# Performance work log

Measured on AMD Instinct MI355X. Metric: run time of the kernel, lower is better.

The kernel has to match this reference:

```python
import jax, jax.numpy as jnp
import numpy as np

N = 50000   # nodes (single node type)
E = 200000  # edges per relation
R = 2       # relations (etypes)
D = 256     # in_dim == out_dim
H = 8       # heads
DK = D // H # 32
SQRT_DK = float(np.sqrt(DK))


def setup_inputs() -> dict:
    key = jax.random.key(0)
    ks = jax.random.split(key, 12)
    wsc = 1.0 / np.sqrt(D)   # linear-layer scale
    rsc = 1.0 / np.sqrt(DK)  # xavier-ish scale for relation tensors
    return {
        "x": jax.random.normal(ks[0], (N, D), jnp.float32),
        "src": jax.random.randint(ks[1], (R, E), 0, N, jnp.int32),
        "dst": jax.random.randint(ks[2], (R, E), 0, N, jnp.int32),
        "Wk": jax.random.normal(ks[3], (D, D), jnp.float32) * wsc,
        "bk": jnp.zeros((D,), jnp.float32),
        "Wq": jax.random.normal(ks[4], (D, D), jnp.float32) * wsc,
        "bq": jnp.zeros((D,), jnp.float32),
        "Wv": jax.random.normal(ks[5], (D, D), jnp.float32) * wsc,
        "bv": jnp.zeros((D,), jnp.float32),
        "Wa": jax.random.normal(ks[6], (D, D), jnp.float32) * wsc,
        "ba": jnp.zeros((D,), jnp.float32),
        "rel_pri": jnp.ones((R, H), jnp.float32),
        "rel_att": jax.random.normal(ks[7], (R, H, DK, DK), jnp.float32) * rsc,
        "rel_msg": jax.random.normal(ks[8], (R, H, DK, DK), jnp.float32) * rsc,
        "skip": jnp.ones((1,), jnp.float32),
    }


def reference(x, src, dst, Wk, bk, Wq, bq, Wv, bv, Wa, ba, rel_pri, rel_att, rel_msg, skip):
    # Per-type K/Q/V projections (single node type) -> [N,H,DK]
    k = (x @ Wk + bk).reshape(N, H, DK)
    q = (x @ Wq + bq).reshape(N, H, DK)
    v = (x @ Wv + bv).reshape(N, H, DK)

    # edge_attention: per-relation bmm transform of gathered src features
    key_t = jnp.einsum('rehd,rhdf->rehf', k[src], rel_att)   # [R,E,H,DK]
    val = jnp.einsum('rehd,rhdf->rehf', v[src], rel_msg)     # [R,E,H,DK]
    att = (q[dst] * key_t).sum(-1) * rel_pri[:, None, :] / SQRT_DK  # [R,E,H]

    # segment softmax over incoming edges per (relation, dst node)
    seg = (dst + N * jnp.arange(R, dtype=dst.dtype)[:, None]).reshape(-1)  # [R*E]
    att_f = att.reshape(R * E, H)
    m = jax.ops.segment_max(att_f, seg, num_segments=R * N)
    m = jnp.where(jnp.isfinite(m), m, 0.0)  # empty segments -> never gathered
    e = jnp.exp(att_f - m[seg])
    den = jax.ops.segment_sum(e, seg, num_segments=R * N)
    attn = e / den[seg]                                       # [R*E,H]

    # weighted-sum scatter aggregation, then cross_reducer='mean' over relations
    h = jax.ops.segment_sum(attn[:, :, None] * val.reshape(R * E, H, DK), seg,
                            num_segments=R * N)               # [R*N,H,DK]
    t = h.reshape(R, N, D).mean(axis=0)                        # [N,D]

    # skip-gated output projection (dropout inactive in eval, use_norm=False)
    alpha = jax.nn.sigmoid(skip[0])
    return (t @ Wa + ba) * alpha + x * (1.0 - alpha)
```

## Files before the change

### kernel.cpp

```cpp
#include <hip/hip_runtime.h>
#include <hip/hip_bf16.h>
#include <math.h>

#define NN 50000
#define EE 200000
#define DD 256
#define HH 8
#define DKK 32
#define NSEG (2 * NN)
#define SCAN_BLOCKS ((NSEG + 1023) / 1024)
#define MPAD 50048
#define LDQKV 1280
#define CAST_BLOCKS 12500

constexpr float RSQRT_DK = 0.17677669529663687f;

__device__ __forceinline__ float bf_lo(unsigned u) { return __uint_as_float(u << 16); }
__device__ __forceinline__ float bf_hi(unsigned u) { return __uint_as_float(u & 0xffff0000u); }
__device__ __forceinline__ unsigned short f2bf(float f) {
    unsigned u = __float_as_uint(f);
    return (unsigned short)((u + 0x7fffu + ((u >> 16) & 1u)) >> 16);
}

typedef __attribute__((ext_vector_type(8))) short bf16x8;
typedef __attribute__((ext_vector_type(4))) float f32x4;

#define GLDS16(g, l)                                                                   \
    __builtin_amdgcn_global_load_lds((const __attribute__((address_space(1))) unsigned int*)(g), \
                                     (__attribute__((address_space(3))) unsigned int*)(l), 16, 0, 0)

__global__ void prep_kernel(const float* __restrict__ x, unsigned short* __restrict__ xb,
                            const float* __restrict__ Wq, const float* __restrict__ Wk,
                            const float* __restrict__ Wv, const float* __restrict__ bq,
                            const float* __restrict__ bk, const float* __restrict__ bv,
                            const float* __restrict__ rel_att, const float* __restrict__ rel_msg,
                            const float* __restrict__ Wa, unsigned short* __restrict__ wa_t,
                            unsigned short* __restrict__ Wt, float* __restrict__ bb) {
    if (blockIdx.x < CAST_BLOCKS) {
        const size_t i = ((size_t)blockIdx.x * 256 + threadIdx.x) * 4;
        float4 v = *(const float4*)&x[i];
        ushort4 o;
        o.x = f2bf(v.x); o.y = f2bf(v.y); o.z = f2bf(v.z); o.w = f2bf(v.w);
        *(ushort4*)&xb[i] = o;
        return;
    }
    const int n = blockIdx.x - CAST_BLOCKS, kk = threadIdx.x;
    if (n >= 1280) {
        const int nn = n - 1280;
        wa_t[(size_t)nn * 256 + kk] = f2bf(Wa[(size_t)kk * 256 + nn]);
        return;
    }
    if (n < 256) {
        Wt[(size_t)n * 256 + kk] = f2bf(Wq[(size_t)kk * 256 + n]);
        if (kk == 0) bb[n] = bq[n];
        return;
    }
    const int sec = (n - 256) >> 8;
    const int c = (n - 256) & 255;
    const int h = c >> 5, f = c & 31;
    const float* W    = (sec < 2) ? Wk : Wv;
    const float* bsrc = (sec < 2) ? bk : bv;
    const float* T = ((sec < 2) ? rel_att : rel_msg)
                   + (size_t)(sec & 1) * HH * DKK * DKK + (size_t)h * DKK * DKK + f;
    const float* wrow = &W[(size_t)kk * 256 + h * 32];
    float s = 0.f;
    #pragma unroll
    for (int d = 0; d < 32; ++d) s += wrow[d] * T[(size_t)d * 32];
    Wt[(size_t)n * 256 + kk] = f2bf(s);
    if (kk == 0) {
        float sb = 0.f;
        for (int d = 0; d < 32; ++d) sb += bsrc[h * 32 + d] * T[(size_t)d * 32];
        bb[n] = sb;
    }
}

__global__ __launch_bounds__(256) void mfma_gemm(
        const unsigned short* __restrict__ A, const unsigned short* __restrict__ Bt,
        const float* __restrict__ bias,
        unsigned short* __restrict__ Cbf, float* __restrict__ Cf,
        int M, int ldc, const float* __restrict__ xres, const float* __restrict__ skip) {
    __shared__ __align__(16) unsigned short As[3][8][64][8];
    __shared__ __align__(16) unsigned short Bs[3][8][64][8];
    const int t = threadIdx.x;
    const int w = t >> 6, l = t & 63;

    const int nwg = gridDim.x * gridDim.y;
    int lin = blockIdx.y * gridDim.x + blockIdx.x;
    {
        const int xcd = lin & 7, pos = lin >> 3;
        const int q = nwg >> 3, r = nwg & 7;
        lin = (xcd < r ? xcd * (q + 1) : r * (q + 1) + (xcd - r) * q) + pos;
    }
    const int n0 = (lin % gridDim.x) * 128;
    const int m0 = (lin / gridDim.x) * 128;
    const int wm = w & 1, wn = w >> 1;

    const int sr = l & 15, sq = l >> 4;
    const unsigned short* ga0 = A  + (size_t)(m0 + w * 16 + sr) * 256 + sq * 8;
    const unsigned short* ga1 = A  + (size_t)(m0 + (w + 4) * 16 + sr) * 256 + sq * 8;
    const unsigned short* gb0 = Bt + (size_t)(n0 + w * 16 + sr) * 256 + sq * 8;
    const unsigned short* gb1 = Bt + (size_t)(n0 + (w + 4) * 16 + sr) * 256 + sq * 8;

#define STAGE(buf, k0) do {                    \
        GLDS16(ga0 + (k0), &As[buf][w][0][0]); \
        GLDS16(ga1 + (k0), &As[buf][w + 4][0][0]); \
        GLDS16(gb0 + (k0), &Bs[buf][w][0][0]); \
        GLDS16(gb1 + (k0), &Bs[buf][w + 4][0][0]); } while (0)

    f32x4 acc[4][4];
    #pragma unroll
    for (int mi = 0; mi < 4; ++mi)
        #pragma unroll
        for (int ni = 0; ni < 4; ++ni) acc[mi][ni] = (f32x4){0.f, 0.f, 0.f, 0.f};

    STAGE(0, 0);
    STAGE(1, 32);
    #pragma unroll
    for (int it = 0; it < 8; ++it) {
        if (it < 7) { asm volatile("s_waitcnt vmcnt(4)" ::: "memory"); }
        else        { asm volatile("s_waitcnt vmcnt(0)" ::: "memory"); }
        __builtin_amdgcn_s_barrier();
        __builtin_amdgcn_sched_barrier(0);
        if (it < 6) {
            STAGE((it + 2) % 3, (it + 2) * 32);
        }
        const int b = it % 3;
        bf16x8 af[4], bfr[4];
        #pragma unroll
        for (int i = 0; i < 4; ++i) {
            af[i]  = *(const bf16x8*)&As[b][wm * 4 + i][l][0];
            bfr[i] = *(const bf16x8*)&Bs[b][wn * 4 + i][l][0];
        }
        #pragma unroll
        for (int mi = 0; mi < 4; ++mi)
            #pragma unroll
            for (int ni = 0; ni < 4; ++ni)
                acc[mi][ni] = __builtin_amdgcn_mfma_f32_16x16x32_bf16(af[mi], bfr[ni],
                                                                      acc[mi][ni], 0, 0, 0);
    }
    __syncthreads();

    unsigned short* ep = (w < 2) ? &As[0][0][0][0] : &Bs[0][0][0][0];
    ep += (w & 1) * 4096;
    const int q4 = l >> 4, c15 = l & 15;

    if (Cf == nullptr) {
        #pragma unroll
        for (int ni = 0; ni < 4; ++ni) {
            const float bcol = bias[n0 + wn * 64 + ni * 16 + c15];
            const int g = ni * 2 + (c15 >> 3);
            #pragma unroll
            for (int mi = 0; mi < 4; ++mi)
                #pragma unroll
                for (int p = 0; p < 4; ++p) {
                    const int row = mi * 16 + q4 * 4 + p;
                    ep[row * 64 + ((g ^ (row & 7)) << 3) + (c15 & 7)] =
                        f2bf(acc[mi][ni][p] + bcol);
                }
        }
        __syncthreads();
        const int rs = l >> 3, cc = l & 7;
        #pragma unroll
        for (int i = 0; i < 8; ++i) {
            const int rl = i * 8 + rs;
            const int row = m0 + wm * 64 + rl;
            if (row < M) {
                uint4 v = *(const uint4*)&ep[rl * 64 + ((cc ^ (rl & 7)) << 3)];
                *(uint4*)&Cbf[(size_t)row * (size_t)ldc + n0 + wn * 64 + cc * 8] = v;
            }
        }
    } else {
        const float alpha = 1.f / (1.f + __expf(-skip[0]));
        const float beta = 1.f - alpha;
        float* epf = (float*)ep;
        #pragma unroll
        for (int half = 0; half < 2; ++half) {
            __syncthreads();
            #pragma unroll
            for (int mi2 = 0; mi2 < 2; ++mi2) {
                const int mi = half * 2 + mi2;
                #pragma unroll
                for (int ni = 0; ni < 4; ++ni) {
                    const float bcol = bias[n0 + wn * 64 + ni * 16 + c15];
                    const int g = ni * 4 + (c15 >> 2);
                    #pragma unroll
                    for (int p = 0; p < 4; ++p) {
                        const int row = mi2 * 16 + q4 * 4 + p;
                        epf[row * 64 + ((g ^ (row & 7)) << 2) + (c15 & 3)] =
                            acc[mi][ni][p] + bcol;
                    }
                }
            }
            __syncthreads();
            const int cc = l & 15, rs = l >> 4;
            #pragma unroll
            for (int i = 0; i < 8; ++i) {
                const int rl = i * 4 + rs;
                const int row = m0 + wm * 64 + half * 32 + rl;
                if (row < M) {
                    const int col = n0 + wn * 64 + cc * 4;
                    float4 v = *(const float4*)&epf[rl * 64 + ((cc ^ (rl & 7)) << 2)];
                    float4 xr = *(const float4*)&xres[(size_t)row * 256 + col];
                    v.x = v.x * alpha + xr.x * beta;
                    v.y = v.y * alpha + xr.y * beta;
                    v.z = v.z * alpha + xr.z * beta;
                    v.w = v.w * alpha + xr.w * beta;
                    *(float4*)&Cf[(size_t)row * 256 + col] = v;
                }
            }
        }
    }
#undef STAGE
}

__global__ void count_kernel(const int* __restrict__ dst, int* __restrict__ cnt) {
    int e = blockIdx.x * 256 + threadIdx.x;
    if (e < 2 * EE) atomicAdd(&cnt[(e / EE) * NN + dst[e]], 1);
}

__global__ __launch_bounds__(1024) void scan_local_kernel(const int* __restrict__ cnt,
                                                          int* __restrict__ rowptr,
                                                          int* __restrict__ bsum) {
    __shared__ int sh[1024];
    const int t = threadIdx.x;
    const int idx = blockIdx.x * 1024 + t;
    const int c = (idx < NSEG) ? cnt[idx] : 0;
    sh[t] = c;
    __syncthreads();
    #pragma unroll
    for (int ofs = 1; ofs < 1024; ofs <<= 1) {
        int v = (t >= ofs) ? sh[t - ofs] : 0;
        __syncthreads();
        sh[t] += v;
        __syncthreads();
    }
    if (idx < NSEG) rowptr[idx] = sh[t] - c;
    if (t == 1023) bsum[blockIdx.x] = sh[1023];
}

__global__ __launch_bounds__(1024) void scan_add_kernel(int* __restrict__ rowptr,
                                                        const int* __restrict__ bsum,
                                                        int* __restrict__ cursor) {
    __shared__ int sb[128];
    const int t = threadIdx.x;
    if (t < 128) sb[t] = (t < SCAN_BLOCKS) ? bsum[t] : 0;
    __syncthreads();
    #pragma unroll
    for (int ofs = 1; ofs < 128; ofs <<= 1) {
        int u = 0;
        if (t < 128 && t >= ofs) u = sb[t - ofs];
        __syncthreads();
        if (t < 128) sb[t] += u;
        __syncthreads();
    }
    const int pre = sb[blockIdx.x] - bsum[blockIdx.x];
    const int idx = blockIdx.x * 1024 + t;
    if (idx < NSEG) {
        const int v = rowptr[idx] + pre;
        rowptr[idx] = v;
        cursor[idx] = v;
    }
    if (blockIdx.x == 0 && t == 127) rowptr[NSEG] = sb[127];
}

__global__ void scatter_kernel(const int* __restrict__ src, const int* __restrict__ dst,
                               int* __restrict__ cursor, int* __restrict__ csr_src) {
    int e = blockIdx.x * 256 + threadIdx.x;
    if (e >= 2 * EE) return;
    int seg = (e / EE) * NN + dst[e];
    int pos = atomicAdd(&cursor[seg], 1);
    csr_src[pos] = src[e];
}

__global__ __launch_bounds__(512) void node_agg_kernel(
        const unsigned short* __restrict__ qkv,
        const int* __restrict__ csr_src,
        const int* __restrict__ rowptr,
        const float* __restrict__ pri,
        unsigned short* __restrict__ tt_bf) {
    __shared__ float sh[4][256];
    const int w = threadIdx.x >> 6, lane = threadIdx.x & 63;
    const int nl = w >> 1, r = w & 1;
    const int n = blockIdx.x * 4 + nl;
    const int lh = lane & 31;
    const int eh = lane >> 5;
    const int h = lh >> 2;
    const size_t coff = (size_t)lh * 8;

    const uint4 qv = *(const uint4*)&qkv[(size_t)n * LDQKV + coff];
    const float q0 = bf_lo(qv.x), q1 = bf_hi(qv.x), q2 = bf_lo(qv.y), q3 = bf_hi(qv.y);
    const float q4_ = bf_lo(qv.z), q5 = bf_hi(qv.z), q6 = bf_lo(qv.w), q7 = bf_hi(qv.w);

    const float prm = pri[r * HH + h] * RSQRT_DK;
    const int seg = r * NN + n;
    const int j0 = rowptr[seg], j1 = rowptr[seg + 1];
    const size_t kbase = 256 + (size_t)r * 256 + coff;
    const size_t vbase = 768 + (size_t)r * 256 + coff;

    float a0 = 0.f, a1 = 0.f, a2 = 0.f, a3 = 0.f, a4 = 0.f, a5 = 0.f, a6 = 0.f, a7 = 0.f;
    float den = 0.f;

    int j = j0 + eh;
    uint4 kv, vv;
    bool valid = j < j1;
    if (valid) {
        const size_t rowb = (size_t)csr_src[j] * LDQKV;
        kv = *(const uint4*)&qkv[rowb + kbase];
        vv = *(const uint4*)&qkv[rowb + vbase];
    }
    while (valid) {
        const int jn = j + 2;
        const bool validn = jn < j1;
        uint4 kvn, vvn;
        if (validn) {
            const size_t rowb = (size_t)csr_src[jn] * LDQKV;
            kvn = *(const uint4*)&qkv[rowb + kbase];
            vvn = *(const uint4*)&qkv[rowb + vbase];
        }
        float p = q0 * bf_lo(kv.x) + q1 * bf_hi(kv.x) + q2 * bf_lo(kv.y) + q3 * bf_hi(kv.y)
                + q4_ * bf_lo(kv.z) + q5 * bf_hi(kv.z) + q6 * bf_lo(kv.w) + q7 * bf_hi(kv.w);
        p += __shfl_xor(p, 1);
        p += __shfl_xor(p, 2);
        const float a = __expf(p * prm);
        den += a;
        a0 += a * bf_lo(vv.x); a1 += a * bf_hi(vv.x);
        a2 += a * bf_lo(vv.y); a3 += a * bf_hi(vv.y);
        a4 += a * bf_lo(vv.z); a5 += a * bf_hi(vv.z);
        a6 += a * bf_lo(vv.w); a7 += a * bf_hi(vv.w);
        kv = kvn; vv = vvn; j = jn; valid = validn;
    }
    den += __shfl_xor(den, 32);
    a0 += __shfl_xor(a0, 32); a1 += __shfl_xor(a1, 32);
    a2 += __shfl_xor(a2, 32); a3 += __shfl_xor(a3, 32);
    a4 += __shfl_xor(a4, 32); a5 += __shfl_xor(a5, 32);
    a6 += __shfl_xor(a6, 32); a7 += __shfl_xor(a7, 32);
    const float wgt = (den > 0.f) ? 0.5f / den : 0.f;

    if (r == 0 && eh == 0) {
        sh[nl][0 * 32 + lh] = a0 * wgt; sh[nl][1 * 32 + lh] = a1 * wgt;
        sh[nl][2 * 32 + lh] = a2 * wgt; sh[nl][3 * 32 + lh] = a3 * wgt;
        sh[nl][4 * 32 + lh] = a4 * wgt; sh[nl][5 * 32 + lh] = a5 * wgt;
        sh[nl][6 * 32 + lh] = a6 * wgt; sh[nl][7 * 32 + lh] = a7 * wgt;
    }
    __syncthreads();
    if (r == 1 && eh == 0) {
        const float t0 = sh[nl][0 * 32 + lh] + a0 * wgt;
        const float t1 = sh[nl][1 * 32 + lh] + a1 * wgt;
        const float t2 = sh[nl][2 * 32 + lh] + a2 * wgt;
        const float t3 = sh[nl][3 * 32 + lh] + a3 * wgt;
        const float t4 = sh[nl][4 * 32 + lh] + a4 * wgt;
        const float t5 = sh[nl][5 * 32 + lh] + a5 * wgt;
        const float t6 = sh[nl][6 * 32 + lh] + a6 * wgt;
        const float t7 = sh[nl][7 * 32 + lh] + a7 * wgt;
        uint4 o;
        o.x = (unsigned)f2bf(t0) | ((unsigned)f2bf(t1) << 16);
        o.y = (unsigned)f2bf(t2) | ((unsigned)f2bf(t3) << 16);
        o.z = (unsigned)f2bf(t4) | ((unsigned)f2bf(t5) << 16);
        o.w = (unsigned)f2bf(t6) | ((unsigned)f2bf(t7) << 16);
        *(uint4*)&tt_bf[(size_t)n * 256 + coff] = o;
    }
}

extern "C" void kernel_launch(void* const* d_in, const int* in_sizes, int n_in,
                              void* d_out, int out_size, void* d_ws, size_t ws_size,
                              hipStream_t stream) {
    const float* x       = (const float*)d_in[0];
    const int*   src     = (const int*)d_in[1];
    const int*   dst     = (const int*)d_in[2];
    const float* Wk      = (const float*)d_in[3];
    const float* bk      = (const float*)d_in[4];
    const float* Wq      = (const float*)d_in[5];
    const float* bq      = (const float*)d_in[6];
    const float* Wv      = (const float*)d_in[7];
    const float* bv      = (const float*)d_in[8];
    const float* Wa      = (const float*)d_in[9];
    const float* ba      = (const float*)d_in[10];
    const float* rel_pri = (const float*)d_in[11];
    const float* rel_att = (const float*)d_in[12];
    const float* rel_msg = (const float*)d_in[13];
    const float* skip    = (const float*)d_in[14];
    float* out = (float*)d_out;
    char* ws = (char*)d_ws;

    size_t off = 0;
    unsigned short* x_bf   = (unsigned short*)(ws + off); off += (size_t)MPAD * DD * 2;
    unsigned short* qkv_bf = (unsigned short*)(ws + off); off += (size_t)NN * LDQKV * 2;
    unsigned short* tt_bf  = (unsigned short*)(ws + off); off += (size_t)MPAD * DD * 2;
    unsigned short* wqkv_t = (unsigned short*)(ws + off); off += (size_t)LDQKV * 256 * 2;
    unsigned short* wa_t   = (unsigned short*)(ws + off); off += (size_t)256 * 256 * 2;
    float*          bb     = (float*)(ws + off);          off += LDQKV * 4;
    int*            cnt    = (int*)(ws + off);            off += (size_t)NSEG * 4;
    int*            rowptr = (int*)(ws + off);            off += (size_t)(NSEG + 1) * 4;
    int*            cursor = (int*)(ws + off);            off += (size_t)NSEG * 4;
    int*            bsum   = (int*)(ws + off);            off += 128 * 4;
    int*            csr_src= (int*)(ws + off);            off += (size_t)2 * EE * 4;
    if (ws_size < off) return;

    prep_kernel<<<CAST_BLOCKS + 1536, 256, 0, stream>>>(
        x, x_bf, Wq, Wk, Wv, bq, bk, bv, rel_att, rel_msg, Wa, wa_t, wqkv_t, bb);

    dim3 g_qkv(LDQKV / 128, MPAD / 128);
    mfma_gemm<<<g_qkv, 256, 0, stream>>>(x_bf, wqkv_t, bb, qkv_bf, nullptr,
                                         NN, LDQKV, nullptr, nullptr);

    hipMemsetAsync(cnt, 0, (size_t)NSEG * 4, stream);
    const int eg = (2 * EE + 255) / 256;
    count_kernel<<<eg, 256, 0, stream>>>(dst, cnt);
    scan_local_kernel<<<SCAN_BLOCKS, 1024, 0, stream>>>(cnt, rowptr, bsum);
    scan_add_kernel<<<SCAN_BLOCKS, 1024, 0, stream>>>(rowptr, bsum, cursor);
    scatter_kernel<<<eg, 256, 0, stream>>>(src, dst, cursor, csr_src);

    node_agg_kernel<<<NN / 4, 512, 0, stream>>>(qkv_bf, csr_src, rowptr,
                                                rel_pri, tt_bf);

    dim3 g_out(DD / 128, MPAD / 128);
    mfma_gemm<<<g_out, 256, 0, stream>>>(tt_bf, wa_t, ba, nullptr, out,
                                         NN, DD, x, skip);
}
```

Baseline: 368.2 us.

## Restructure MFMA GEMM to 128x64 tiles with full-K B in LDS and direct A loads

```diff
diff --git a/kernel.cpp b/kernel.cpp
--- a/kernel.cpp
+++ b/kernel.cpp
@@ -74,143 +74,141 @@
     }
 }
 
-__global__ __launch_bounds__(256) void mfma_gemm(
+__global__ __launch_bounds__(256, 4) void mfma_gemm(
         const unsigned short* __restrict__ A, const unsigned short* __restrict__ Bt,
         const float* __restrict__ bias,
         unsigned short* __restrict__ Cbf, float* __restrict__ Cf,
         int M, int ldc, const float* __restrict__ xres, const float* __restrict__ skip) {
-    __shared__ __align__(16) unsigned short As[3][8][64][8];
-    __shared__ __align__(16) unsigned short Bs[3][8][64][8];
+    __shared__ __align__(16) unsigned short Bs[8][4][64][8];
+    __shared__ __align__(16) unsigned short Ep[4][1024];
     const int t = threadIdx.x;
     const int w = t >> 6, l = t & 63;
-
-    const int nwg = gridDim.x * gridDim.y;
-    int lin = blockIdx.y * gridDim.x + blockIdx.x;
+    const int NT = gridDim.x;
+
+    const int nwg = NT * gridDim.y;
+    int lin = blockIdx.y * NT + blockIdx.x;
     {
         const int xcd = lin & 7, pos = lin >> 3;
         const int q = nwg >> 3, r = nwg & 7;
         lin = (xcd < r ? xcd * (q + 1) : r * (q + 1) + (xcd - r) * q) + pos;
     }
-    const int n0 = (lin % gridDim.x) * 128;
-    const int m0 = (lin / gridDim.x) * 128;
-    const int wm = w & 1, wn = w >> 1;
+    const int n0 = (lin % NT) * 64;
+    const int m0 = (lin / NT) * 128;
 
     const int sr = l & 15, sq = l >> 4;
-    const unsigned short* ga0 = A  + (size_t)(m0 + w * 16 + sr) * 256 + sq * 8;
-    const unsigned short* ga1 = A  + (size_t)(m0 + (w + 4) * 16 + sr) * 256 + sq * 8;
-    const unsigned short* gb0 = Bt + (size_t)(n0 + w * 16 + sr) * 256 + sq * 8;
-    const unsigned short* gb1 = Bt + (size_t)(n0 + (w + 4) * 16 + sr) * 256 + sq * 8;
-
-#define STAGE(buf, k0) do {                    \
-        GLDS16(ga0 + (k0), &As[buf][w][0][0]); \
-        GLDS16(ga1 + (k0), &As[buf][w + 4][0][0]); \
-        GLDS16(gb0 + (k0), &Bs[buf][w][0][0]); \
-        GLDS16(gb1 + (k0), &Bs[buf][w + 4][0][0]); } while (0)
-
-    f32x4 acc[4][4];
-    #pragma unroll
-    for (int mi = 0; mi < 4; ++mi)
+
+    const unsigned short* gb = Bt + (size_t)(n0 + w * 16 + sr) * 256 + sq * 8;
+    #pragma unroll
+    for (int kk = 0; kk < 8; ++kk)
+        GLDS16(gb + kk * 32, &Bs[kk][w][0][0]);
+
+    const unsigned short* gaA = A + (size_t)(m0 + w * 32 + sr) * 256 + sq * 8;
+    const unsigned short* gaB = A + (size_t)(m0 + w * 32 + 16 + sr) * 256 + sq * 8;
+
+    asm volatile("s_waitcnt vmcnt(0)" ::: "memory");
+    __builtin_amdgcn_s_barrier();
+
+    f32x4 acc[2][4];
+    #pragma unroll
+    for (int mi = 0; mi < 2; ++mi)
         #pragma unroll
         for (int ni = 0; ni < 4; ++ni) acc[mi][ni] = (f32x4){0.f, 0.f, 0.f, 0.f};
 
-    STAGE(0, 0);
-    STAGE(1, 32);
-    #pragma unroll
-    for (int it = 0; it < 8; ++it) {
-        if (it < 7) { asm volatile("s_waitcnt vmcnt(4)" ::: "memory"); }
-        else        { asm volatile("s_waitcnt vmcnt(0)" ::: "memory"); }
-        __builtin_amdgcn_s_barrier();
-        __builtin_amdgcn_sched_barrier(0);
-        if (it < 6) {
-            STAGE((it + 2) % 3, (it + 2) * 32);
+    bf16x8 a0[2], a1[2];
+    a0[0] = *(const bf16x8*)(gaA);
+    a1[0] = *(const bf16x8*)(gaB);
+    #pragma unroll
+    for (int kk = 0; kk < 8; ++kk) {
+        const int cur = kk & 1, nxt = cur ^ 1;
+        if (kk < 7) {
+            a0[nxt] = *(const bf16x8*)(gaA + (kk + 1) * 32);
+            a1[nxt] = *(const bf16x8*)(gaB + (kk + 1) * 32);
         }
-        const int b = it % 3;
-        bf16x8 af[4], bfr[4];
+        bf16x8 bfr[4];
         #pragma unroll
-        for (int i = 0; i < 4; ++i) {
-            af[i]  = *(const bf16x8*)&As[b][wm * 4 + i][l][0];
-            bfr[i] = *(const bf16x8*)&Bs[b][wn * 4 + i][l][0];
-        }
-        #pragma unroll
-        for (int mi = 0; mi < 4; ++mi)
-            #pragma unroll
-            for (int ni = 0; ni < 4; ++ni)
-                acc[mi][ni] = __builtin_amdgcn_mfma_f32_16x16x32_bf16(af[mi], bfr[ni],
-                                                                      acc[mi][ni], 0, 0, 0);
-    }
-    __syncthreads();
-
-    unsigned short* ep = (w < 2) ? &As[0][0][0][0] : &Bs[0][0][0][0];
-    ep += (w & 1) * 4096;
-    const int q4 = l >> 4, c15 = l & 15;
-
-    if (Cf == nullptr) {
+        for (int ni = 0; ni < 4; ++ni)
+            bfr[ni] = *(const bf16x8*)&Bs[kk][ni][l][0];
         #pragma unroll
         for (int ni = 0; ni < 4; ++ni) {
-            const float bcol = bias[n0 + wn * 64 + ni * 16 + c15];
-            const int g = ni * 2 + (c15 >> 3);
+            acc[0][ni] = __builtin_amdgcn_mfma_f32_16x16x32_bf16(a0[cur], bfr[ni],
+                                                                 acc[0][ni], 0, 0, 0);
+            acc[1][ni] = __builtin_amdgcn_mfma_f32_16x16x32_bf16(a1[cur], bfr[ni],
+                                                                 acc[1][ni], 0, 0, 0);
+        }
+    }
+
+    const int q4 = l >> 4, c15 = l & 15;
+    if (Cf == nullptr) {
+        unsigned short* epw = &Ep[w][0];
+        #pragma unroll
+        for (int mi = 0; mi < 2; ++mi) {
             #pragma unroll
-            for (int mi = 0; mi < 4; ++mi)
+            for (int ni = 0; ni < 4; ++ni) {
+                const float bcol = bias[n0 + ni * 16 + c15];
+                const int g = ni * 2 + (c15 >> 3);
                 #pragma unroll
                 for (int p = 0; p < 4; ++p) {
-                    const int row = mi * 16 + q4 * 4 + p;
-                    ep[row * 64 + ((g ^ (row & 7)) << 3) + (c15 & 7)] =
+                    const int rl = q4 * 4 + p;
+                    epw[rl * 64 + ((g ^ (rl & 7)) << 3) + (c15 & 7)] =
                         f2bf(acc[mi][ni][p] + bcol);
                 }
-        }
-        __syncthreads();
-        const int rs = l >> 3, cc = l & 7;
-        #pragma unroll
-        for (int i = 0; i < 8; ++i) {
-            const int rl = i * 8 + rs;
-            const int row = m0 + wm * 64 + rl;
-            if (row < M) {
-                uint4 v = *(const uint4*)&ep[rl * 64 + ((cc ^ (rl & 7)) << 3)];
-                *(uint4*)&Cbf[(size_t)row * (size_t)ldc + n0 + wn * 64 + cc * 8] = v;
             }
+            asm volatile("s_waitcnt lgkmcnt(0)" ::: "memory");
+            __builtin_amdgcn_sched_barrier(0);
+            const int rs = l >> 3, cc = l & 7;
+            #pragma unroll
+            for (int i = 0; i < 2; ++i) {
+                const int rl = i * 8 + rs;
+                const int row = m0 + w * 32 + mi * 16 + rl;
+                if (row < M) {
+                    uint4 v = *(const uint4*)&epw[rl * 64 + ((cc ^ (rl & 7)) << 3)];
+                    *(uint4*)&Cbf[(size_t)row * (size_t)ldc + n0 + cc * 8] = v;
+                }
+            }
+            __builtin_amdgcn_sched_barrier(0);
         }
     } else {
         const float alpha = 1.f / (1.f + __expf(-skip[0]));
         const float beta = 1.f - alpha;
-        float* epf = (float*)ep;
+        float* epf = (float*)&Ep[w][0];
         #pragma unroll
-        for (int half = 0; half < 2; ++half) {
-            __syncthreads();
+        for (int mi = 0; mi < 2; ++mi) {
             #pragma unroll
-            for (int mi2 = 0; mi2 < 2; ++mi2) {
-                const int mi = half * 2 + mi2;
+            for (int nh = 0; nh < 2; ++nh) {
                 #pragma unroll
-                for (int ni = 0; ni < 4; ++ni) {
-                    const float bcol = bias[n0 + wn * 64 + ni * 16 + c15];
-                    const int g = ni * 4 + (c15 >> 2);
+                for (int ni2 = 0; ni2 < 2; ++ni2) {
+                    const int ni = nh * 2 + ni2;
+                    const float bcol = bias[n0 + ni * 16 + c15];
+                    const int g = ni2 * 4 + (c15 >> 2);
                     #pragma unroll
                     for (int p = 0; p < 4; ++p) {
-                        const int row = mi2 * 16 + q4 * 4 + p;
-                        epf[row * 64 + ((g ^ (row & 7)) << 2) + (c15 & 3)] =
+                        const int rl = q4 * 4 + p;
+                        epf[rl * 32 + ((g ^ (rl & 7)) << 2) + (c15 & 3)] =
                             acc[mi][ni][p] + bcol;
                     }
                 }
-            }
-            __syncthreads();
-            const int cc = l & 15, rs = l >> 4;
-            #pragma unroll
-            for (int i = 0; i < 8; ++i) {
-                const int rl = i * 4 + rs;
-                const int row = m0 + wm * 64 + half * 32 + rl;
-                if (row < M) {
-                    const int col = n0 + wn * 64 + cc * 4;
-                    float4 v = *(const float4*)&epf[rl * 64 + ((cc ^ (rl & 7)) << 2)];
-                    float4 xr = *(const float4*)&xres[(size_t)row * 256 + col];
-                    v.x = v.x * alpha + xr.x * beta;
-                    v.y = v.y * alpha + xr.y * beta;
-                    v.z = v.z * alpha + xr.z * beta;
-                    v.w = v.w * alpha + xr.w * beta;
-                    *(float4*)&Cf[(size_t)row * 256 + col] = v;
+                asm volatile("s_waitcnt lgkmcnt(0)" ::: "memory");
+                __builtin_amdgcn_sched_barrier(0);
+                const int cc = l & 7, rs = l >> 3;
+                #pragma unroll
+                for (int i = 0; i < 2; ++i) {
+                    const int rl = i * 8 + rs;
+                    const int row = m0 + w * 32 + mi * 16 + rl;
+                    if (row < M) {
+                        const int col = n0 + nh * 32 + cc * 4;
+                        float4 v = *(const float4*)&epf[rl * 32 + ((cc ^ (rl & 7)) << 2)];
+                        float4 xr = *(const float4*)&xres[(size_t)row * 256 + col];
+                        v.x = v.x * alpha + xr.x * beta;
+                        v.y = v.y * alpha + xr.y * beta;
+                        v.z = v.z * alpha + xr.z * beta;
+                        v.w = v.w * alpha + xr.w * beta;
+                        *(float4*)&Cf[(size_t)row * 256 + col] = v;
+                    }
                 }
+                __builtin_amdgcn_sched_barrier(0);
             }
         }
     }
-#undef STAGE
 }
 
 __global__ void count_kernel(const int* __restrict__ dst, int* __restrict__ cnt) {
@@ -399,7 +397,7 @@
     prep_kernel<<<CAST_BLOCKS + 1536, 256, 0, stream>>>(
         x, x_bf, Wq, Wk, Wv, bq, bk, bv, rel_att, rel_msg, Wa, wa_t, wqkv_t, bb);
 
-    dim3 g_qkv(LDQKV / 128, MPAD / 128);
+    dim3 g_qkv(LDQKV / 64, MPAD / 128);
     mfma_gemm<<<g_qkv, 256, 0, stream>>>(x_bf, wqkv_t, bb, qkv_bf, nullptr,
                                          NN, LDQKV, nullptr, nullptr);
 
@@ -413,7 +411,7 @@
     node_agg_kernel<<<NN / 4, 512, 0, stream>>>(qkv_bf, csr_src, rowptr,
                                                 rel_pri, tt_bf);
 
-    dim3 g_out(DD / 128, MPAD / 128);
+    dim3 g_out(DD / 64, MPAD / 128);
     mfma_gemm<<<g_out, 256, 0, stream>>>(tt_bf, wa_t, ba, nullptr, out,
                                          NN, DD, x, skip);
 }
```

Result: no change. 373.4 us (+1.4%).
